# Kernel tuning notes

Measured on AMD Instinct MI355X. Metric: run time of the kernel, lower is better.

The kernel has to match this reference:

```python
import jax, jax.numpy as jnp
import numpy as np

N_NODES = 50000
N_EDGES = 800000
D_IN = 128
N_HEAD = 4
D_OUT = D_IN // N_HEAD  # 32


def setup_inputs() -> dict:
    key = jax.random.key(0)
    k1, k2, k3, k4, k5 = jax.random.split(key, 5)
    in_feat = jax.random.normal(k1, (N_NODES, D_IN), dtype=jnp.float32)
    edge_ind = jax.random.randint(k2, (2, N_EDGES), 0, N_NODES, dtype=jnp.int64)
    # xavier-ish scaled params
    W_proj = jax.random.normal(k3, (D_IN, N_HEAD * D_OUT), dtype=jnp.float32) * (1.0 / np.sqrt(D_IN))
    a_src = jax.random.normal(k4, (1, N_HEAD, D_OUT), dtype=jnp.float32) * (1.0 / np.sqrt(D_OUT))
    a_tgt = jax.random.normal(k5, (1, N_HEAD, D_OUT), dtype=jnp.float32) * (1.0 / np.sqrt(D_OUT))
    bias = jnp.zeros((N_HEAD * D_OUT,), dtype=jnp.float32)
    return {"in_feat": in_feat, "edge_ind": edge_ind, "edge_len": N_EDGES,
            "W_proj": W_proj, "a_src": a_src, "a_tgt": a_tgt, "bias": bias}


def reference(in_feat, edge_ind, edge_len, W_proj, a_src, a_tgt, bias):
    n_nodes = in_feat.shape[0]
    n_head, d_out = a_src.shape[1], a_src.shape[2]
    # input projection: [N, d_in] @ [d_in, H*D] -> [N, H, D]
    proj_feat = (in_feat @ W_proj).reshape(n_nodes, n_head, d_out)
    # per-node scores [N, H]
    src_score = jnp.sum(proj_feat * a_src, axis=-1)
    tgt_score = jnp.sum(proj_feat * a_tgt, axis=-1)
    src_ind, tgt_ind = edge_ind[0], edge_ind[1]
    # per-edge score [E, H]
    edge_score = jax.nn.leaky_relu(src_score[src_ind] + tgt_score[tgt_ind], negative_slope=0.2)
    edge_score = jnp.exp(edge_score - jnp.max(edge_score))  # global max, as in source
    # segment-softmax denominator via scatter-add over target nodes
    neigh_sums = jax.ops.segment_sum(edge_score, tgt_ind, num_segments=n_nodes)  # [N, H]
    att_per_edge = edge_score / (neigh_sums[tgt_ind] + 1e-16)  # [E, H]
    # weighted aggregation: gather src features, scale, scatter-add to targets
    src_feat_weighted = proj_feat[src_ind] * att_per_edge[..., None]  # [E, H, D]
    out_feat = jax.ops.segment_sum(src_feat_weighted, tgt_ind, num_segments=n_nodes)  # [N, H, D]
    return out_feat.reshape(n_nodes, -1) + bias
```

## Files before the change

kernel.cpp:

```cpp
#include <hip/hip_runtime.h>
#include <hip/hip_bf16.h>

typedef __attribute__((ext_vector_type(8))) short bf16x8;
typedef __attribute__((ext_vector_type(4))) float f32x4;

__device__ __forceinline__ ushort f2bf(float f) {
    unsigned u = __float_as_uint(f);
    return (ushort)((u + 0x7fffu + ((u >> 16) & 1u)) >> 16);
}
__device__ __forceinline__ float blo(unsigned u) { return __uint_as_float(u << 16); }
__device__ __forceinline__ float bhi(unsigned u) { return __uint_as_float(u & 0xffff0000u); }

__global__ void k_wt(const float* __restrict__ W, ushort* __restrict__ Wt,
                     int* __restrict__ deg, int n) {
    int idx = blockIdx.x * 256 + threadIdx.x;
    if (idx < 16384) {
        int nn = idx >> 7, kk = idx & 127;
        Wt[idx] = f2bf(W[kk * 128 + nn]);
    }
    if (idx < n) deg[idx] = 0;
}

__global__ __launch_bounds__(256) void k_proj(const float* __restrict__ A,
                                              const ushort* __restrict__ Wt_g,
                                              const float* __restrict__ a_src,
                                              const float* __restrict__ a_tgt,
                                              ushort* __restrict__ Pb,
                                              float* __restrict__ ss,
                                              float* __restrict__ ts, int n) {
    __shared__ __align__(16) char smem[49152];
    const int tid = threadIdx.x;
    const int row0 = blockIdx.x * 64;

#pragma unroll
    for (int it = 0; it < 8; ++it) {
        int idx = it * 256 + tid;
        int r   = idx >> 5;
        int kc  = (idx & 31) << 2;
        int gr  = row0 + r;
        float4 v = make_float4(0.f, 0.f, 0.f, 0.f);
        if (gr < n) v = *(const float4*)&A[(size_t)gr * 128 + kc];
        ushort4 pk;
        pk.x = f2bf(v.x); pk.y = f2bf(v.y); pk.z = f2bf(v.z); pk.w = f2bf(v.w);
        *(ushort4*)(smem + ((r * 256 + kc * 2) ^ ((r & 7) << 4))) = pk;
    }
#pragma unroll
    for (int it = 0; it < 8; ++it) {
        int idx = it * 256 + tid;
        int nn  = idx >> 4;
        int k8  = (idx & 15) << 3;
        uint4 v = *(const uint4*)&Wt_g[nn * 128 + k8];
        *(uint4*)(smem + 16384 + ((nn * 256 + k8 * 2) ^ ((nn & 7) << 4))) = v;
    }
    __syncthreads();

    const int l  = tid & 63, w = tid >> 6;
    const int lr = l & 15,  lk = l >> 4;
    const int arow = w * 16 + lr;

    f32x4 acc[8] = {};
#pragma unroll
    for (int ks = 0; ks < 4; ++ks) {
        int kk = ks * 32 + lk * 8;
        bf16x8 af = *(const bf16x8*)(smem + ((arow * 256 + kk * 2) ^ ((arow & 7) << 4)));
#pragma unroll
        for (int nt = 0; nt < 8; ++nt) {
            int nn = nt * 16 + lr;
            bf16x8 bf = *(const bf16x8*)(smem + 16384 + ((nn * 256 + kk * 2) ^ ((nn & 7) << 4)));
            acc[nt] = __builtin_amdgcn_mfma_f32_16x16x32_bf16(af, bf, acc[nt], 0, 0, 0);
        }
    }

#pragma unroll
    for (int nt = 0; nt < 8; ++nt) {
#pragma unroll
        for (int r = 0; r < 4; ++r) {
            int gr = row0 + w * 16 + lk * 4 + r;
            if (gr < n) Pb[(size_t)gr * 128 + nt * 16 + lr] = f2bf(acc[nt][r]);
        }
    }

    float av[8], bw[8];
#pragma unroll
    for (int t = 0; t < 8; ++t) { av[t] = a_src[t * 16 + lr]; bw[t] = a_tgt[t * 16 + lr]; }
#pragma unroll
    for (int r = 0; r < 4; ++r) {
#pragma unroll
        for (int h = 0; h < 4; ++h) {
            float s1 = acc[2 * h][r] * av[2 * h] + acc[2 * h + 1][r] * av[2 * h + 1];
            float s2 = acc[2 * h][r] * bw[2 * h] + acc[2 * h + 1][r] * bw[2 * h + 1];
#pragma unroll
            for (int off = 1; off < 16; off <<= 1) {
                s1 += __shfl_xor(s1, off, 64);
                s2 += __shfl_xor(s2, off, 64);
            }
            if (lr == 0) {
                int gr = row0 + w * 16 + lk * 4 + r;
                if (gr < n) { ss[gr * 4 + h] = s1; ts[gr * 4 + h] = s2; }
            }
        }
    }
}

__global__ void k_hist(const int* __restrict__ tgt, int* __restrict__ deg,
                       ushort* __restrict__ rank, int E) {
    int e = blockIdx.x * 256 + threadIdx.x;
    if (e < E) rank[e] = (ushort)atomicAdd(&deg[tgt[e]], 1);
}

__global__ __launch_bounds__(256) void k_scan1(const int* __restrict__ deg,
                                               int* __restrict__ rowptr,
                                               int* __restrict__ sums, int n) {
    __shared__ int sd[256];
    int tid = threadIdx.x;
    int i = blockIdx.x * 256 + tid;
    int v = (i < n) ? ((deg[i] + 3) & ~3) : 0;
    sd[tid] = v; __syncthreads();
#pragma unroll
    for (int off = 1; off < 256; off <<= 1) {
        int t = (tid >= off) ? sd[tid - off] : 0;
        __syncthreads();
        sd[tid] += t;
        __syncthreads();
    }
    if (i < n) rowptr[i + 1] = sd[tid];
    if (tid == 255) sums[blockIdx.x] = sd[255];
}

__global__ __launch_bounds__(256) void k_scan23(int* __restrict__ rowptr,
                                                const int* __restrict__ sums,
                                                int nchunks, int n) {
    __shared__ int sd[256];
    int tid = threadIdx.x;
    int v = (tid < nchunks) ? sums[tid] : 0;
    sd[tid] = v; __syncthreads();
#pragma unroll
    for (int off = 1; off < 256; off <<= 1) {
        int t = (tid >= off) ? sd[tid - off] : 0;
        __syncthreads();
        sd[tid] += t;
        __syncthreads();
    }
    int b = blockIdx.x;
    int prefix = (b == 0) ? 0 : sd[b - 1];
    int i = b * 256 + tid;
    if (i < n) {
        rowptr[i + 1] += prefix;
        if (i == 0) rowptr[0] = 0;
    }
}

__global__ void k_scatter(const int* __restrict__ src, const int* __restrict__ tgt,
                          const int* __restrict__ rowptr, const ushort* __restrict__ rank,
                          const int* __restrict__ deg, ushort* __restrict__ srcs,
                          int E, int n) {
    int e = blockIdx.x * 256 + threadIdx.x;
    if (e < E) {
        int t = tgt[e];
        srcs[rowptr[t] + rank[e]] = (ushort)src[e];
    } else {
        int i = e - E;
        if (i < n) {
            int j  = rowptr[i] + deg[i];
            int j1 = rowptr[i + 1];
            for (; j < j1; ++j) srcs[j] = 0xFFFFu;
        }
    }
}

__global__ __launch_bounds__(256) void k_aggr(const int* __restrict__ rowptr,
                                              const ushort* __restrict__ srcs,
                                              const float* __restrict__ ss,
                                              const float* __restrict__ ts,
                                              const ushort* __restrict__ Pb,
                                              const float* __restrict__ bias,
                                              float* __restrict__ out, int n) {
    int node = __builtin_amdgcn_readfirstlane(blockIdx.x * 4 + (threadIdx.x >> 6));
    if (node >= n) return;
    const int lane = threadIdx.x & 63;
    const int c = lane * 2;
    const int h = lane >> 4;
    const float tsc = ts[node * 4 + h];
    const int b0 = rowptr[node], b1 = rowptr[node + 1];

    float ax0 = 0.f, ay0 = 0.f, ax1 = 0.f, ay1 = 0.f;
    float ax2 = 0.f, ay2 = 0.f, ax3 = 0.f, ay3 = 0.f;
    float den = 0.f;

    for (int i = b0; i < b1; i += 8) {
        uint2 ka = *(const uint2*)(srcs + i);
        uint2 kb;
        if (i + 4 < b1) kb = *(const uint2*)(srcs + i + 4);
        else            kb = make_uint2(0xFFFFFFFFu, 0xFFFFFFFFu);
        int s0 = ka.x & 0xFFFF, s1 = ka.x >> 16, s2 = ka.y & 0xFFFF, s3 = ka.y >> 16;
        int s4 = kb.x & 0xFFFF, s5 = kb.x >> 16, s6 = kb.y & 0xFFFF, s7 = kb.y >> 16;
        bool v0 = s0 < n, v1 = s1 < n, v2 = s2 < n, v3 = s3 < n;
        bool v4 = s4 < n, v5 = s5 < n, v6 = s6 < n, v7 = s7 < n;
        int m0 = v0 ? s0 : 0, m1 = v1 ? s1 : 0, m2 = v2 ? s2 : 0, m3 = v3 ? s3 : 0;
        int m4 = v4 ? s4 : 0, m5 = v5 ? s5 : 0, m6 = v6 ? s6 : 0, m7 = v7 ? s7 : 0;
        unsigned p0 = *(const unsigned*)(Pb + (size_t)m0 * 128 + c);
        unsigned p1 = *(const unsigned*)(Pb + (size_t)m1 * 128 + c);
        unsigned p2 = *(const unsigned*)(Pb + (size_t)m2 * 128 + c);
        unsigned p3 = *(const unsigned*)(Pb + (size_t)m3 * 128 + c);
        unsigned p4 = *(const unsigned*)(Pb + (size_t)m4 * 128 + c);
        unsigned p5 = *(const unsigned*)(Pb + (size_t)m5 * 128 + c);
        unsigned p6 = *(const unsigned*)(Pb + (size_t)m6 * 128 + c);
        unsigned p7 = *(const unsigned*)(Pb + (size_t)m7 * 128 + c);
        float sc0 = ss[m0 * 4 + h], sc1 = ss[m1 * 4 + h];
        float sc2 = ss[m2 * 4 + h], sc3 = ss[m3 * 4 + h];
        float sc4 = ss[m4 * 4 + h], sc5 = ss[m5 * 4 + h];
        float sc6 = ss[m6 * 4 + h], sc7 = ss[m7 * 4 + h];
        sc0 = v0 ? sc0 : -1e30f; sc1 = v1 ? sc1 : -1e30f;
        sc2 = v2 ? sc2 : -1e30f; sc3 = v3 ? sc3 : -1e30f;
        sc4 = v4 ? sc4 : -1e30f; sc5 = v5 ? sc5 : -1e30f;
        sc6 = v6 ? sc6 : -1e30f; sc7 = v7 ? sc7 : -1e30f;
        float w0 = sc0 + tsc; w0 = w0 > 0.f ? w0 : 0.2f * w0;  float e0 = __expf(w0);
        float w1 = sc1 + tsc; w1 = w1 > 0.f ? w1 : 0.2f * w1;  float e1 = __expf(w1);
        float w2 = sc2 + tsc; w2 = w2 > 0.f ? w2 : 0.2f * w2;  float e2 = __expf(w2);
        float w3 = sc3 + tsc; w3 = w3 > 0.f ? w3 : 0.2f * w3;  float e3 = __expf(w3);
        float w4 = sc4 + tsc; w4 = w4 > 0.f ? w4 : 0.2f * w4;  float e4 = __expf(w4);
        float w5 = sc5 + tsc; w5 = w5 > 0.f ? w5 : 0.2f * w5;  float e5 = __expf(w5);
        float w6 = sc6 + tsc; w6 = w6 > 0.f ? w6 : 0.2f * w6;  float e6 = __expf(w6);
        float w7 = sc7 + tsc; w7 = w7 > 0.f ? w7 : 0.2f * w7;  float e7 = __expf(w7);
        den += ((e0 + e1) + (e2 + e3)) + ((e4 + e5) + (e6 + e7));
        ax0 = fmaf(e0, blo(p0), ax0); ay0 = fmaf(e0, bhi(p0), ay0);
        ax1 = fmaf(e1, blo(p1), ax1); ay1 = fmaf(e1, bhi(p1), ay1);
        ax2 = fmaf(e2, blo(p2), ax2); ay2 = fmaf(e2, bhi(p2), ay2);
        ax3 = fmaf(e3, blo(p3), ax3); ay3 = fmaf(e3, bhi(p3), ay3);
        ax0 = fmaf(e4, blo(p4), ax0); ay0 = fmaf(e4, bhi(p4), ay0);
        ax1 = fmaf(e5, blo(p5), ax1); ay1 = fmaf(e5, bhi(p5), ay1);
        ax2 = fmaf(e6, blo(p6), ax2); ay2 = fmaf(e6, bhi(p6), ay2);
        ax3 = fmaf(e7, blo(p7), ax3); ay3 = fmaf(e7, bhi(p7), ay3);
    }
    float inv = 1.f / (den + 1e-16f);
    float2 bv = *(const float2*)&bias[c];
    float2 o;
    o.x = ((ax0 + ax1) + (ax2 + ax3)) * inv + bv.x;
    o.y = ((ay0 + ay1) + (ay2 + ay3)) * inv + bv.y;
    *(float2*)&out[(size_t)node * 128 + c] = o;
}

extern "C" void kernel_launch(void* const* d_in, const int* in_sizes, int n_in,
                              void* d_out, int out_size, void* d_ws, size_t ws_size,
                              hipStream_t stream) {
    const float* in_feat = (const float*)d_in[0];
    const int*   edge    = (const int*)d_in[1];
    const float* W_proj  = (const float*)d_in[3];
    const float* a_src   = (const float*)d_in[4];
    const float* a_tgt   = (const float*)d_in[5];
    const float* bias    = (const float*)d_in[6];
    float* out = (float*)d_out;

    const int n = in_sizes[0] / 128;
    const int E = in_sizes[1] / 2;
    const int* src = edge;
    const int* tgt = edge + E;

    ushort* Pb   = (ushort*)d_ws;
    ushort* Wt_g = Pb + (size_t)n * 128;
    float*  ss   = (float*)(Wt_g + 128 * 128);
    float*  ts   = ss + (size_t)n * 4;
    int* deg    = (int*)(ts + (size_t)n * 4);
    int* rowptr = deg + n;
    int* sums   = rowptr + n + 1;
    ushort* rank = (ushort*)(sums + 256);
    ushort* srcs = rank + E;

    const int nchunks = (n + 255) / 256;

    k_wt<<<(n + 255) / 256, 256, 0, stream>>>(W_proj, Wt_g, deg, n);
    k_hist<<<(E + 255) / 256, 256, 0, stream>>>(tgt, deg, rank, E);
    k_proj<<<(n + 63) / 64, 256, 0, stream>>>(in_feat, Wt_g, a_src, a_tgt,
                                              Pb, ss, ts, n);
    k_scan1<<<nchunks, 256, 0, stream>>>(deg, rowptr, sums, n);
    k_scan23<<<nchunks, 256, 0, stream>>>(rowptr, sums, nchunks, n);
    k_scatter<<<(E + n + 255) / 256, 256, 0, stream>>>(src, tgt, rowptr, rank,
                                                       deg, srcs, E, n);
    k_aggr<<<(n + 3) / 4, 256, 0, stream>>>(rowptr, srcs, ss, ts, Pb, bias, out, n);
}
```

Baseline: 115.1 us.

## Fuse histogram into projection launch and shard CSR scatter by address

Merges the degree histogram into the projection kernel as extra blocks, so the atomic-heavy histogram can run alongside the GEMM blocks instead of in a separate launch. Splits the CSR scatter into a position pass and an 8-way sharded scatter. In the sharded scatter, each block rereads a 2048-edge chunk but writes only positions whose 64-byte region matches its shard. The sharding is meant to improve write locality and reduce partial-line contention, at the cost of reading pos and src eight times and adding an extra kernel plus a pos buffer. The workspace layout is also reorganised with 16-byte aligned allocations.

```diff
diff --git a/kernel.cpp b/kernel.cpp
--- a/kernel.cpp
+++ b/kernel.cpp
@@ -21,15 +21,26 @@
     if (idx < n) deg[idx] = 0;
 }
 
-__global__ __launch_bounds__(256) void k_proj(const float* __restrict__ A,
-                                              const ushort* __restrict__ Wt_g,
-                                              const float* __restrict__ a_src,
-                                              const float* __restrict__ a_tgt,
-                                              ushort* __restrict__ Pb,
-                                              float* __restrict__ ss,
-                                              float* __restrict__ ts, int n) {
+__global__ __launch_bounds__(256) void k_projhist(const float* __restrict__ A,
+                                                  const ushort* __restrict__ Wt_g,
+                                                  const float* __restrict__ a_src,
+                                                  const float* __restrict__ a_tgt,
+                                                  ushort* __restrict__ Pb,
+                                                  float* __restrict__ ss,
+                                                  float* __restrict__ ts,
+                                                  const int* __restrict__ tgt,
+                                                  int* __restrict__ deg,
+                                                  ushort* __restrict__ rank,
+                                                  int n, int E, int PB) {
     __shared__ __align__(16) char smem[49152];
     const int tid = threadIdx.x;
+
+    if ((int)blockIdx.x >= PB) {
+        int e = ((int)blockIdx.x - PB) * 256 + tid;
+        if (e < E) rank[e] = (ushort)atomicAdd(&deg[tgt[e]], 1);
+        return;
+    }
+
     const int row0 = blockIdx.x * 64;
 
 #pragma unroll
@@ -102,12 +113,6 @@
     }
 }
 
-__global__ void k_hist(const int* __restrict__ tgt, int* __restrict__ deg,
-                       ushort* __restrict__ rank, int E) {
-    int e = blockIdx.x * 256 + threadIdx.x;
-    if (e < E) rank[e] = (ushort)atomicAdd(&deg[tgt[e]], 1);
-}
-
 __global__ __launch_bounds__(256) void k_scan1(const int* __restrict__ deg,
                                                int* __restrict__ rowptr,
                                                int* __restrict__ sums, int n) {
@@ -150,20 +155,33 @@
     }
 }
 
-__global__ void k_scatter(const int* __restrict__ src, const int* __restrict__ tgt,
-                          const int* __restrict__ rowptr, const ushort* __restrict__ rank,
-                          const int* __restrict__ deg, ushort* __restrict__ srcs,
-                          int E, int n) {
+__global__ void k_pos(const int* __restrict__ tgt, const int* __restrict__ rowptr,
+                      const ushort* __restrict__ rank, const int* __restrict__ deg,
+                      int* __restrict__ pos, ushort* __restrict__ srcs, int E, int n) {
     int e = blockIdx.x * 256 + threadIdx.x;
     if (e < E) {
-        int t = tgt[e];
-        srcs[rowptr[t] + rank[e]] = (ushort)src[e];
+        pos[e] = rowptr[tgt[e]] + rank[e];
     } else {
         int i = e - E;
         if (i < n) {
             int j  = rowptr[i] + deg[i];
             int j1 = rowptr[i + 1];
             for (; j < j1; ++j) srcs[j] = 0xFFFFu;
+        }
+    }
+}
+
+__global__ __launch_bounds__(256) void k_scatter(const int* __restrict__ src,
+                                                 const int* __restrict__ pos,
+                                                 ushort* __restrict__ srcs, int E) {
+    const int shard = blockIdx.x & 7;
+    const int base  = (blockIdx.x >> 3) * 2048;
+#pragma unroll
+    for (int j = 0; j < 8; ++j) {
+        int e = base + j * 256 + threadIdx.x;
+        if (e < E) {
+            int p = pos[e];
+            if (((p >> 5) & 7) == shard) srcs[p] = (ushort)src[e];
         }
     }
 }
@@ -256,25 +274,33 @@
     const int* src = edge;
     const int* tgt = edge + E;
 
-    ushort* Pb   = (ushort*)d_ws;
-    ushort* Wt_g = Pb + (size_t)n * 128;
-    float*  ss   = (float*)(Wt_g + 128 * 128);
-    float*  ts   = ss + (size_t)n * 4;
-    int* deg    = (int*)(ts + (size_t)n * 4);
-    int* rowptr = deg + n;
-    int* sums   = rowptr + n + 1;
-    ushort* rank = (ushort*)(sums + 256);
-    ushort* srcs = rank + E;
+    uintptr_t p = (uintptr_t)d_ws;
+    auto alloc = [&](size_t bytes) { uintptr_t r = p; p = (p + bytes + 15) & ~(uintptr_t)15; return r; };
+    float*  ss     = (float*)alloc((size_t)n * 4 * 4);
+    float*  ts     = (float*)alloc((size_t)n * 4 * 4);
+    int*    deg    = (int*)alloc((size_t)n * 4);
+    int*    rowptr = (int*)alloc((size_t)(n + 1) * 4);
+    int*    sums   = (int*)alloc(256 * 4);
+    ushort* Pb     = (ushort*)alloc((size_t)n * 128 * 2);
+    ushort* Wt_g   = (ushort*)alloc(16384 * 2);
+    ushort* rank   = (ushort*)alloc((size_t)E * 2);
+    int*    pos    = (int*)alloc((size_t)E * 4);
+    ushort* srcs   = (ushort*)alloc(((size_t)E + 4 * (size_t)n + 8) * 2);
 
     const int nchunks = (n + 255) / 256;
+    const int PB = (n + 63) / 64;
+    const int HB = (E + 255) / 256;
 
     k_wt<<<(n + 255) / 256, 256, 0, stream>>>(W_proj, Wt_g, deg, n);
-    k_hist<<<(E + 255) / 256, 256, 0, stream>>>(tgt, deg, rank, E);
-    k_proj<<<(n + 63) / 64, 256, 0, stream>>>(in_feat, Wt_g, a_src, a_tgt,
-                                              Pb, ss, ts, n);
+    k_projhist<<<PB + HB, 256, 0, stream>>>(in_feat, Wt_g, a_src, a_tgt,
+                                            Pb, ss, ts, tgt, deg, rank, n, E, PB);
     k_scan1<<<nchunks, 256, 0, stream>>>(deg, rowptr, sums, n);
     k_scan23<<<nchunks, 256, 0, stream>>>(rowptr, sums, nchunks, n);
-    k_scatter<<<(E + n + 255) / 256, 256, 0, stream>>>(src, tgt, rowptr, rank,
-                                                       deg, srcs, E, n);
+    k_pos<<<(E + n + 255) / 256, 256, 0, stream>>>(tgt, rowptr, rank, deg,
+                                                   pos, srcs, E, n);
+    {
+        int chunks = (E + 2047) / 2048;
+        k_scatter<<<chunks * 8, 256, 0, stream>>>(src, pos, srcs, E);
+    }
     k_aggr<<<(n + 3) / 4, 256, 0, stream>>>(rowptr, srcs, ss, ts, Pb, bias, out, n);
 }
```

Measured after the change: 122.4 us. 1.06x slower.
